# Optimization experiments

Hardware: AMD Instinct MI355X
Metric: run time of the kernel (lower is better)

Reference implementation:

```python
import jax, jax.numpy as jnp
import numpy as np

DIM = 1024
NUM_HEADS = 16
HEAD_DIM = DIM // NUM_HEADS
SCALE = HEAD_DIM ** -0.5
B, S = 2, 2048


def setup_inputs() -> dict:
    key = jax.random.key(0)
    ks = jax.random.split(key, 5)
    inv = 1.0 / np.sqrt(DIM)  # mimic nn.Linear init scale
    return {
        "query": jax.random.normal(ks[0], (B, S, DIM), dtype=jnp.float32),
        "Wq": jax.random.normal(ks[1], (DIM, DIM), dtype=jnp.float32) * inv,
        "Wk": jax.random.normal(ks[2], (DIM, DIM), dtype=jnp.float32) * inv,
        "Wv": jax.random.normal(ks[3], (DIM, DIM), dtype=jnp.float32) * inv,
        "Wo": jax.random.normal(ks[4], (DIM, DIM), dtype=jnp.float32) * inv,
    }


def reference(query, Wq, Wk, Wv, Wo):
    # nn.Linear(dim, dim, bias=False): y = x @ W.T  (W is [out, in])
    Q = query @ Wq.T  # [B, S, D]
    K = query @ Wk.T
    V = query @ Wv.T
    # split heads: [B, H, S, hd]
    def split(x):
        return x.reshape(B, S, NUM_HEADS, HEAD_DIM).transpose(0, 2, 1, 3)
    Qh, Kh, Vh = split(Q), split(K), split(V)
    scores = jnp.einsum("bhqd,bhkd->bhqk", Qh, Kh) * SCALE  # [B,H,Sq,Sk]
    probs = jax.nn.softmax(scores, axis=-1)
    attn = jnp.einsum("bhqk,bhkd->bhqd", probs, Vh)  # [B,H,Sq,hd]
    attn = attn.transpose(0, 2, 1, 3).reshape(B, S, DIM)
    return attn @ Wo.T
```

## Files before the change

kernel.cpp:

```cpp
#include <hip/hip_runtime.h>
#include <hip/hip_bf16.h>


#define DIMK   1024
#define NHEADS 16
#define HDIM   64
#define BATCH  2
#define SEQ    2048
#define MTOT   (BATCH*SEQ)

typedef __attribute__((ext_vector_type(8))) short bf16x8;
typedef __attribute__((ext_vector_type(4))) float f32x4;

__device__ __forceinline__ void gl16(const void* g, void* l) {
  __builtin_amdgcn_global_load_lds((const __attribute__((address_space(1))) void*)g,
                                   (__attribute__((address_space(3))) void*)l, 16, 0, 0);
}

__device__ __forceinline__ unsigned short f2bf(float f) {
  union { float f; unsigned int u; } a; a.f = f;
  unsigned int r = a.u + 0x7fffu + ((a.u >> 16) & 1u);
  return (unsigned short)(r >> 16);
}
__device__ __forceinline__ float bf2f(unsigned short h) {
  union { unsigned int u; float f; } a; a.u = ((unsigned int)h) << 16;
  return a.f;
}
__device__ __forceinline__ void split2(float v, unsigned short& hi, unsigned short& lo) {
  hi = f2bf(v);
  lo = f2bf(v - bf2f(hi));
}

__global__ __launch_bounds__(256) void convert_kernel(
    const float* __restrict__ X, const float* __restrict__ Wq,
    const float* __restrict__ Wk, const float* __restrict__ Wv,
    const float* __restrict__ Wo,
    unsigned short* __restrict__ Xhi, unsigned short* __restrict__ Xlo,
    unsigned short* __restrict__ Whi, unsigned short* __restrict__ Wlo,
    unsigned short* __restrict__ Wohi, unsigned short* __restrict__ Wolo)
{
  const int NX4 = MTOT * DIMK / 4;
  const int NW4 = DIMK * DIMK / 4;
  int id = blockIdx.x * blockDim.x + threadIdx.x;
  const float4* s; unsigned short* dh; unsigned short* dl; int si, di;
  if (id < NX4) { s = (const float4*)X; si = id; di = id; dh = Xhi; dl = Xlo; }
  else if (id < NX4 + 3 * NW4) {
    int t = id - NX4; di = t;
    if (t < NW4)          { s = (const float4*)Wq; si = t; }
    else if (t < 2 * NW4) { s = (const float4*)Wk; si = t - NW4; }
    else                  { s = (const float4*)Wv; si = t - 2 * NW4; }
    dh = Whi; dl = Wlo;
  } else {
    int t = id - NX4 - 3 * NW4; s = (const float4*)Wo; si = t; di = t; dh = Wohi; dl = Wolo;
  }
  float4 v = s[si];
  ushort4 hi, lo;
  split2(v.x, hi.x, lo.x); split2(v.y, hi.y, lo.y);
  split2(v.z, hi.z, lo.z); split2(v.w, hi.w, lo.w);
  ((ushort4*)dh)[di] = hi;
  ((ushort4*)dl)[di] = lo;
}

__device__ __forceinline__ void gemm_mainloop(
    const unsigned short* __restrict__ Ahi, const unsigned short* __restrict__ Alo,
    const unsigned short* __restrict__ Bhi, const unsigned short* __restrict__ Blo,
    int m0, int n0, int K, unsigned short* As, unsigned short* Bs, f32x4 acc[4][4])
{
  int tid = threadIdx.x; int w = tid >> 6; int l = tid & 63;
  int wm = w >> 1, wn = w & 1, lr = l & 15, lg = l >> 4;
  for (int kk = 0; kk < K; kk += 32) {
#pragma unroll
    for (int it = 0; it < 2; ++it) {
      int c = it * 256 + w * 64 + l;
      int row = c >> 2, col = (c & 3) * 8;
      int lb = (it * 256 + w * 64) * 8;
      gl16(Ahi + (long)(m0 + row) * K + kk + col, As + lb);
      gl16(Alo + (long)(m0 + row) * K + kk + col, As + 4096 + lb);
      gl16(Bhi + (long)(n0 + row) * K + kk + col, Bs + lb);
      gl16(Blo + (long)(n0 + row) * K + kk + col, Bs + 4096 + lb);
    }
    __syncthreads();
    bf16x8 ah[4], al[4], bh[4], bl[4];
#pragma unroll
    for (int i = 0; i < 4; i++) {
      int ra = (wm * 64 + i * 16 + lr) * 32 + lg * 8;
      ah[i] = *(const bf16x8*)(As + ra);
      al[i] = *(const bf16x8*)(As + 4096 + ra);
      int rb = (wn * 64 + i * 16 + lr) * 32 + lg * 8;
      bh[i] = *(const bf16x8*)(Bs + rb);
      bl[i] = *(const bf16x8*)(Bs + 4096 + rb);
    }
#pragma unroll
    for (int mi = 0; mi < 4; mi++)
#pragma unroll
      for (int ni = 0; ni < 4; ni++) {
        acc[mi][ni] = __builtin_amdgcn_mfma_f32_16x16x32_bf16(ah[mi], bh[ni], acc[mi][ni], 0, 0, 0);
        acc[mi][ni] = __builtin_amdgcn_mfma_f32_16x16x32_bf16(ah[mi], bl[ni], acc[mi][ni], 0, 0, 0);
        acc[mi][ni] = __builtin_amdgcn_mfma_f32_16x16x32_bf16(al[mi], bh[ni], acc[mi][ni], 0, 0, 0);
      }
    __syncthreads();
  }
}

__global__ __launch_bounds__(256) void gemm_qkv_kernel(
    const unsigned short* __restrict__ Xhi, const unsigned short* __restrict__ Xlo,
    const unsigned short* __restrict__ Whi, const unsigned short* __restrict__ Wlo,
    unsigned short* __restrict__ Qhi, unsigned short* __restrict__ Qlo,
    unsigned short* __restrict__ Khi, unsigned short* __restrict__ Klo,
    unsigned short* __restrict__ Vthi, unsigned short* __restrict__ Vtlo)
{
  __shared__ __align__(16) unsigned short As[2 * 4096];
  __shared__ __align__(16) unsigned short Bs[2 * 4096];
  int m0 = blockIdx.y * 128, n0 = blockIdx.x * 128;
  f32x4 acc[4][4] = {};
  gemm_mainloop(Xhi, Xlo, Whi, Wlo, m0, n0, DIMK, As, Bs, acc);
  int tid = threadIdx.x; int w = tid >> 6, l = tid & 63;
  int wm = w >> 1, wn = w & 1, lr = l & 15, lg = l >> 4;
  int sec = n0 >> 10;
  int nl = (n0 & 1023) + wn * 64;
#pragma unroll
  for (int mi = 0; mi < 4; mi++) {
    int rbase = m0 + wm * 64 + mi * 16 + lg * 4;
#pragma unroll
    for (int ni = 0; ni < 4; ni++) {
      int col = nl + ni * 16 + lr;
      if (sec == 2) {
        ushort4 hi4, lo4;
        split2(acc[mi][ni][0], hi4.x, lo4.x);
        split2(acc[mi][ni][1], hi4.y, lo4.y);
        split2(acc[mi][ni][2], hi4.z, lo4.z);
        split2(acc[mi][ni][3], hi4.w, lo4.w);
        *(ushort4*)(Vthi + (long)col * MTOT + rbase) = hi4;
        *(ushort4*)(Vtlo + (long)col * MTOT + rbase) = lo4;
      } else {
        unsigned short* dh = (sec == 0) ? Qhi : Khi;
        unsigned short* dl = (sec == 0) ? Qlo : Klo;
        float sc = (sec == 0) ? 0.125f : 1.0f;
#pragma unroll
        for (int r = 0; r < 4; r++) {
          float v = acc[mi][ni][r] * sc;
          unsigned short h_, l_;
          split2(v, h_, l_);
          dh[(long)(rbase + r) * DIMK + col] = h_;
          dl[(long)(rbase + r) * DIMK + col] = l_;
        }
      }
    }
  }
}

__global__ __launch_bounds__(256) void attn_kernel(
    const unsigned short* __restrict__ Qhi, const unsigned short* __restrict__ Qlo,
    const unsigned short* __restrict__ Khi, const unsigned short* __restrict__ Klo,
    const unsigned short* __restrict__ Vthi, const unsigned short* __restrict__ Vtlo,
    unsigned short* __restrict__ Ahi, unsigned short* __restrict__ Alo)
{
  __shared__ __align__(16) unsigned short Ks[2 * 4096];
  __shared__ __align__(16) unsigned short Vs[2 * 4096];
  __shared__ __align__(16) unsigned short Ps[2 * 4096];
  int tid = threadIdx.x, w = tid >> 6, l = tid & 63, lr = l & 15, lg = l >> 4;
  int q0 = blockIdx.x * 64;
  int bh = blockIdx.y, b = bh >> 4, h = bh & 15;
  long rowbase = (long)b * SEQ;
  const float L2E = 1.44269504088896340736f;

  bf16x8 qh[2], ql[2];
#pragma unroll
  for (int ks = 0; ks < 2; ks++) {
    long g = (rowbase + q0 + w * 16 + lr) * DIMK + h * HDIM + ks * 32 + lg * 8;
    qh[ks] = *(const bf16x8*)(Qhi + g);
    ql[ks] = *(const bf16x8*)(Qlo + g);
  }
  f32x4 o[4] = {};
  float mrow[4] = { -1e30f, -1e30f, -1e30f, -1e30f };
  float lsum[4] = { 0.f, 0.f, 0.f, 0.f };

  for (int kt = 0; kt < SEQ / 64; kt++) {
#pragma unroll
    for (int it = 0; it < 2; it++) {
      int c = it * 256 + w * 64 + l;
      int row = c >> 3;
      int col = ((c & 7) ^ (row & 7)) * 8;
      int lb = (it * 256 + w * 64) * 8;
      long gk = (rowbase + kt * 64 + row) * DIMK + h * HDIM + col;
      gl16(Khi + gk, Ks + lb);
      gl16(Klo + gk, Ks + 4096 + lb);
      long gv = (long)(h * HDIM + row) * MTOT + rowbase + kt * 64 + col;
      gl16(Vthi + gv, Vs + lb);
      gl16(Vtlo + gv, Vs + 4096 + lb);
    }
    __syncthreads();

    f32x4 s[4] = {};
    __builtin_amdgcn_s_setprio(1);
#pragma unroll
    for (int n = 0; n < 4; n++) {
#pragma unroll
      for (int ks = 0; ks < 2; ks++) {
        int kr = n * 16 + lr;
        int rb = kr * 64 + (((ks * 4 + lg) ^ (kr & 7)) * 8);
        bf16x8 kbh = *(const bf16x8*)(Ks + rb);
        bf16x8 kbl = *(const bf16x8*)(Ks + 4096 + rb);
        s[n] = __builtin_amdgcn_mfma_f32_16x16x32_bf16(qh[ks], kbh, s[n], 0, 0, 0);
        s[n] = __builtin_amdgcn_mfma_f32_16x16x32_bf16(qh[ks], kbl, s[n], 0, 0, 0);
        s[n] = __builtin_amdgcn_mfma_f32_16x16x32_bf16(ql[ks], kbh, s[n], 0, 0, 0);
      }
    }
    __builtin_amdgcn_s_setprio(0);

#pragma unroll
    for (int r = 0; r < 4; r++) {
      float mx = fmaxf(fmaxf(s[0][r], s[1][r]), fmaxf(s[2][r], s[3][r]));
#pragma unroll
      for (int msk = 1; msk < 16; msk <<= 1) mx = fmaxf(mx, __shfl_xor(mx, msk));
      float mnew = fmaxf(mrow[r], mx);
      float alpha = exp2f((mrow[r] - mnew) * L2E);
      float rs = 0.f;
      int qr = w * 16 + lg * 4 + r;
#pragma unroll
      for (int n = 0; n < 4; n++) {
        float p = exp2f((s[n][r] - mnew) * L2E);
        rs += p;
        unsigned short h_, l_;
        split2(p, h_, l_);
        int addr = qr * 64 + ((n * 16 + lr) ^ ((qr & 7) << 3));
        Ps[addr] = h_; Ps[4096 + addr] = l_;
      }
#pragma unroll
      for (int msk = 1; msk < 16; msk <<= 1) rs += __shfl_xor(rs, msk);
      lsum[r] = lsum[r] * alpha + rs;
      mrow[r] = mnew;
      o[0][r] *= alpha; o[1][r] *= alpha; o[2][r] *= alpha; o[3][r] *= alpha;
    }

    __builtin_amdgcn_s_setprio(1);
#pragma unroll
    for (int ks = 0; ks < 2; ks++) {
      int qr = w * 16 + lr;
      int pa = qr * 64 + ((ks * 32 + lg * 8) ^ ((qr & 7) << 3));
      bf16x8 ph = *(const bf16x8*)(Ps + pa);
      bf16x8 pl = *(const bf16x8*)(Ps + 4096 + pa);
#pragma unroll
      for (int nd = 0; nd < 4; nd++) {
        int vr = nd * 16 + lr;
        int vb = vr * 64 + (((ks * 4 + lg) ^ (vr & 7)) * 8);
        bf16x8 vh = *(const bf16x8*)(Vs + vb);
        bf16x8 vl = *(const bf16x8*)(Vs + 4096 + vb);
        o[nd] = __builtin_amdgcn_mfma_f32_16x16x32_bf16(ph, vh, o[nd], 0, 0, 0);
        o[nd] = __builtin_amdgcn_mfma_f32_16x16x32_bf16(ph, vl, o[nd], 0, 0, 0);
        o[nd] = __builtin_amdgcn_mfma_f32_16x16x32_bf16(pl, vh, o[nd], 0, 0, 0);
      }
    }
    __builtin_amdgcn_s_setprio(0);
    __syncthreads();
  }

#pragma unroll
  for (int nd = 0; nd < 4; nd++) {
#pragma unroll
    for (int r = 0; r < 4; r++) {
      long row = rowbase + q0 + w * 16 + lg * 4 + r;
      int col = h * HDIM + nd * 16 + lr;
      float v = o[nd][r] / lsum[r];
      unsigned short h_, l_;
      split2(v, h_, l_);
      Ahi[row * DIMK + col] = h_;
      Alo[row * DIMK + col] = l_;
    }
  }
}

__global__ __launch_bounds__(256) void gemm_out_kernel(
    const unsigned short* __restrict__ Ahi_, const unsigned short* __restrict__ Alo_,
    const unsigned short* __restrict__ Wohi, const unsigned short* __restrict__ Wolo,
    float* __restrict__ out)
{
  __shared__ __align__(16) unsigned short As[2 * 4096];
  __shared__ __align__(16) unsigned short Bs[2 * 4096];
  int m0 = blockIdx.y * 128, n0 = blockIdx.x * 128;
  f32x4 acc[4][4] = {};
  gemm_mainloop(Ahi_, Alo_, Wohi, Wolo, m0, n0, DIMK, As, Bs, acc);
  int tid = threadIdx.x; int w = tid >> 6, l = tid & 63;
  int wm = w >> 1, wn = w & 1, lr = l & 15, lg = l >> 4;
#pragma unroll
  for (int mi = 0; mi < 4; mi++) {
    int rbase = m0 + wm * 64 + mi * 16 + lg * 4;
#pragma unroll
    for (int ni = 0; ni < 4; ni++) {
      int col = n0 + wn * 64 + ni * 16 + lr;
#pragma unroll
      for (int r = 0; r < 4; r++)
        out[(long)(rbase + r) * DIMK + col] = acc[mi][ni][r];
    }
  }
}

extern "C" void kernel_launch(void* const* d_in, const int* in_sizes, int n_in,
                              void* d_out, int out_size, void* d_ws, size_t ws_size,
                              hipStream_t stream)
{
  const float* X  = (const float*)d_in[0];
  const float* Wq = (const float*)d_in[1];
  const float* Wk = (const float*)d_in[2];
  const float* Wv = (const float*)d_in[3];
  const float* Wo = (const float*)d_in[4];
  float* out = (float*)d_out;
  char* ws = (char*)d_ws;
  const size_t MB = 1u << 20;
  unsigned short* Xhi  = (unsigned short*)(ws + 0 * MB);
  unsigned short* Xlo  = (unsigned short*)(ws + 8 * MB);
  unsigned short* Whi  = (unsigned short*)(ws + 16 * MB);
  unsigned short* Wlo  = (unsigned short*)(ws + 22 * MB);
  unsigned short* Wohi = (unsigned short*)(ws + 28 * MB);
  unsigned short* Wolo = (unsigned short*)(ws + 30 * MB);
  unsigned short* Qhi  = (unsigned short*)(ws + 32 * MB);
  unsigned short* Qlo  = (unsigned short*)(ws + 40 * MB);
  unsigned short* Khi  = (unsigned short*)(ws + 48 * MB);
  unsigned short* Klo  = (unsigned short*)(ws + 56 * MB);
  unsigned short* Vthi = (unsigned short*)(ws + 64 * MB);
  unsigned short* Vtlo = (unsigned short*)(ws + 72 * MB);
  unsigned short* AThi = Xhi;
  unsigned short* ATlo = Xlo;

  convert_kernel<<<8192, 256, 0, stream>>>(X, Wq, Wk, Wv, Wo, Xhi, Xlo, Whi, Wlo, Wohi, Wolo);
  gemm_qkv_kernel<<<dim3(24, 32), 256, 0, stream>>>(Xhi, Xlo, Whi, Wlo,
                                                    Qhi, Qlo, Khi, Klo, Vthi, Vtlo);
  attn_kernel<<<dim3(32, 32), 256, 0, stream>>>(Qhi, Qlo, Khi, Klo, Vthi, Vtlo, AThi, ATlo);
  gemm_out_kernel<<<dim3(8, 32), 256, 0, stream>>>(AThi, ATlo, Wohi, Wolo, out);
}
```

Before: 418.5 us.

## Double-buffer K/V tiles in attention and fold log2e into Q scale

The attention kernel now keeps two LDS buffers for K and V and issues the next tile's async global-to-LDS loads before computing on the current tile, so load latency can overlap MFMA and softmax work. The log2(e) factor moves into the Q projection scale, which removes a multiply per exponent, and the hi part of the probability split now truncates instead of rounding. The final normalisation computes one reciprocal per row instead of a divide per element. The costs are more LDS per block, which may lower occupancy, and slightly different rounding.

```diff
diff --git a/kernel.cpp b/kernel.cpp
--- a/kernel.cpp
+++ b/kernel.cpp
@@ -28,6 +28,11 @@
 }
 __device__ __forceinline__ void split2(float v, unsigned short& hi, unsigned short& lo) {
   hi = f2bf(v);
+  lo = f2bf(v - bf2f(hi));
+}
+__device__ __forceinline__ void split2t(float v, unsigned short& hi, unsigned short& lo) {
+  union { float f; unsigned int u; } a; a.f = v;
+  hi = (unsigned short)(a.u >> 16);
   lo = f2bf(v - bf2f(hi));
 }
 
@@ -135,7 +140,7 @@
       } else {
         unsigned short* dh = (sec == 0) ? Qhi : Khi;
         unsigned short* dl = (sec == 0) ? Qlo : Klo;
-        float sc = (sec == 0) ? 0.125f : 1.0f;
+        float sc = (sec == 0) ? (0.125f * 1.44269504088896340736f) : 1.0f;
 #pragma unroll
         for (int r = 0; r < 4; r++) {
           float v = acc[mi][ni][r] * sc;
@@ -155,14 +160,13 @@
     const unsigned short* __restrict__ Vthi, const unsigned short* __restrict__ Vtlo,
     unsigned short* __restrict__ Ahi, unsigned short* __restrict__ Alo)
 {
-  __shared__ __align__(16) unsigned short Ks[2 * 4096];
-  __shared__ __align__(16) unsigned short Vs[2 * 4096];
+  __shared__ __align__(16) unsigned short Ks[2][2 * 4096];
+  __shared__ __align__(16) unsigned short Vs[2][2 * 4096];
   __shared__ __align__(16) unsigned short Ps[2 * 4096];
   int tid = threadIdx.x, w = tid >> 6, l = tid & 63, lr = l & 15, lg = l >> 4;
   int q0 = blockIdx.x * 64;
   int bh = blockIdx.y, b = bh >> 4, h = bh & 15;
   long rowbase = (long)b * SEQ;
-  const float L2E = 1.44269504088896340736f;
 
   bf16x8 qh[2], ql[2];
 #pragma unroll
@@ -175,7 +179,7 @@
   float mrow[4] = { -1e30f, -1e30f, -1e30f, -1e30f };
   float lsum[4] = { 0.f, 0.f, 0.f, 0.f };
 
-  for (int kt = 0; kt < SEQ / 64; kt++) {
+  auto stage = [&](int kt, int buf) {
 #pragma unroll
     for (int it = 0; it < 2; it++) {
       int c = it * 256 + w * 64 + l;
@@ -183,13 +187,24 @@
       int col = ((c & 7) ^ (row & 7)) * 8;
       int lb = (it * 256 + w * 64) * 8;
       long gk = (rowbase + kt * 64 + row) * DIMK + h * HDIM + col;
-      gl16(Khi + gk, Ks + lb);
-      gl16(Klo + gk, Ks + 4096 + lb);
+      gl16(Khi + gk, Ks[buf] + lb);
+      gl16(Klo + gk, Ks[buf] + 4096 + lb);
       long gv = (long)(h * HDIM + row) * MTOT + rowbase + kt * 64 + col;
-      gl16(Vthi + gv, Vs + lb);
-      gl16(Vtlo + gv, Vs + 4096 + lb);
-    }
-    __syncthreads();
+      gl16(Vthi + gv, Vs[buf] + lb);
+      gl16(Vtlo + gv, Vs[buf] + 4096 + lb);
+    }
+  };
+
+  stage(0, 0);
+  __syncthreads();
+
+  const int NT = SEQ / 64;
+  for (int kt = 0; kt < NT; kt++) {
+    int cur = kt & 1;
+    if (kt + 1 < NT) stage(kt + 1, cur ^ 1);
+
+    const unsigned short* Kb = Ks[cur];
+    const unsigned short* Vb = Vs[cur];
 
     f32x4 s[4] = {};
     __builtin_amdgcn_s_setprio(1);
@@ -199,8 +214,8 @@
       for (int ks = 0; ks < 2; ks++) {
         int kr = n * 16 + lr;
         int rb = kr * 64 + (((ks * 4 + lg) ^ (kr & 7)) * 8);
-        bf16x8 kbh = *(const bf16x8*)(Ks + rb);
-        bf16x8 kbl = *(const bf16x8*)(Ks + 4096 + rb);
+        bf16x8 kbh = *(const bf16x8*)(Kb + rb);
+        bf16x8 kbl = *(const bf16x8*)(Kb + 4096 + rb);
         s[n] = __builtin_amdgcn_mfma_f32_16x16x32_bf16(qh[ks], kbh, s[n], 0, 0, 0);
         s[n] = __builtin_amdgcn_mfma_f32_16x16x32_bf16(qh[ks], kbl, s[n], 0, 0, 0);
         s[n] = __builtin_amdgcn_mfma_f32_16x16x32_bf16(ql[ks], kbh, s[n], 0, 0, 0);
@@ -214,15 +229,15 @@
 #pragma unroll
       for (int msk = 1; msk < 16; msk <<= 1) mx = fmaxf(mx, __shfl_xor(mx, msk));
       float mnew = fmaxf(mrow[r], mx);
-      float alpha = exp2f((mrow[r] - mnew) * L2E);
+      float alpha = exp2f(mrow[r] - mnew);
       float rs = 0.f;
       int qr = w * 16 + lg * 4 + r;
 #pragma unroll
       for (int n = 0; n < 4; n++) {
-        float p = exp2f((s[n][r] - mnew) * L2E);
+        float p = exp2f(s[n][r] - mnew);
         rs += p;
         unsigned short h_, l_;
-        split2(p, h_, l_);
+        split2t(p, h_, l_);
         int addr = qr * 64 + ((n * 16 + lr) ^ ((qr & 7) << 3));
         Ps[addr] = h_; Ps[4096 + addr] = l_;
       }
@@ -244,8 +259,8 @@
       for (int nd = 0; nd < 4; nd++) {
         int vr = nd * 16 + lr;
         int vb = vr * 64 + (((ks * 4 + lg) ^ (vr & 7)) * 8);
-        bf16x8 vh = *(const bf16x8*)(Vs + vb);
-        bf16x8 vl = *(const bf16x8*)(Vs + 4096 + vb);
+        bf16x8 vh = *(const bf16x8*)(Vb + vb);
+        bf16x8 vl = *(const bf16x8*)(Vb + 4096 + vb);
         o[nd] = __builtin_amdgcn_mfma_f32_16x16x32_bf16(ph, vh, o[nd], 0, 0, 0);
         o[nd] = __builtin_amdgcn_mfma_f32_16x16x32_bf16(ph, vl, o[nd], 0, 0, 0);
         o[nd] = __builtin_amdgcn_mfma_f32_16x16x32_bf16(pl, vh, o[nd], 0, 0, 0);
@@ -256,12 +271,13 @@
   }
 
 #pragma unroll
-  for (int nd = 0; nd < 4; nd++) {
-#pragma unroll
-    for (int r = 0; r < 4; r++) {
+  for (int r = 0; r < 4; r++) {
+    float inv = 1.0f / lsum[r];
+#pragma unroll
+    for (int nd = 0; nd < 4; nd++) {
       long row = rowbase + q0 + w * 16 + lg * 4 + r;
       int col = h * HDIM + nd * 16 + lr;
-      float v = o[nd][r] / lsum[r];
+      float v = o[nd][r] * inv;
       unsigned short h_, l_;
       split2(v, h_, l_);
       Ahi[row * DIMK + col] = h_;
```

Result: no change. 416.7 us (-0.4%).
